# Optimization experiments

Hardware: AMD Instinct MI355X
Metric: run time of the kernel (lower is better)

The kernel has to match this reference:

```python
import jax, jax.numpy as jnp
import numpy as np

N_NODES = 50000
N_EDGES = 800000
D_IN, D_HID, D_OUT = 128, 256, 128
N_EXPERT = 8


def mean_aggr(x, src, dst, n):
    # scatter-mean of neighbor features onto destination nodes
    msg = x[src]                                            # [E, d]
    s = jax.ops.segment_sum(msg, dst, num_segments=n)       # [N, d]
    cnt = jax.ops.segment_sum(jnp.ones((src.shape[0],), x.dtype), dst, num_segments=n)
    return s / jnp.clip(cnt, 1.0)[:, None]


def moe_top1(x, wg, bg, we, be):
    # FMoE with naive gate, top_k=1: combine weight softmax over top-1 == 1.0
    logits = x @ wg + bg                                    # [N, E]
    gate_full = jax.nn.softmax(logits, axis=-1)             # [N, E]
    idx = jnp.argmax(logits, axis=-1)                       # [N]
    n_expert = we.shape[0]
    out = jnp.zeros((x.shape[0], we.shape[2]), x.dtype)
    for e in range(n_expert):                               # small fixed loop over experts
        mask = (idx == e)[:, None].astype(x.dtype)
        out = out + mask * (x @ we[e] + be[e])
    return out, gate_full


def mysage_conv(x, src, dst, wg, bg, we, be, wr):
    agg = mean_aggr(x, src, dst, x.shape[0])
    out, gate = moe_top1(agg, wg, bg, we, be)
    out = out + x @ wr                                      # root weight (no bias)
    gstd = jnp.std(gate, axis=1, ddof=1).mean()             # torch.std is unbiased
    return out, gstd


def plain_sage_conv(x, src, dst, wl, bl, wr):
    agg = mean_aggr(x, src, dst, x.shape[0])
    return agg @ wl + bl + x @ wr


def setup_inputs() -> dict:
    key = jax.random.key(0)
    ks = jax.random.split(key, 16)
    s = 0.05
    inp = {
        "x": jax.random.normal(ks[0], (N_NODES, D_IN), jnp.float32),
        "edge_index": jax.random.randint(ks[1], (2, N_EDGES), 0, N_NODES, jnp.int64),
        # layer 1 (in -> hid)
        "wg1": jax.random.normal(ks[2], (D_IN, N_EXPERT), jnp.float32) * s,
        "bg1": jnp.zeros((N_EXPERT,), jnp.float32),
        "we1": jax.random.normal(ks[3], (N_EXPERT, D_IN, D_HID), jnp.float32) * s,
        "be1": jnp.zeros((N_EXPERT, D_HID), jnp.float32),
        "wr1": jax.random.normal(ks[4], (D_IN, D_HID), jnp.float32) * s,
        # layer 2 (hid -> hid)
        "wg2": jax.random.normal(ks[5], (D_HID, N_EXPERT), jnp.float32) * s,
        "bg2": jnp.zeros((N_EXPERT,), jnp.float32),
        "we2": jax.random.normal(ks[6], (N_EXPERT, D_HID, D_HID), jnp.float32) * s,
        "be2": jnp.zeros((N_EXPERT, D_HID), jnp.float32),
        "wr2": jax.random.normal(ks[7], (D_HID, D_HID), jnp.float32) * s,
        # layer 3 plain SAGEConv (hid -> out)
        "wl3": jax.random.normal(ks[8], (D_HID, D_OUT), jnp.float32) * s,
        "bl3": jnp.zeros((D_OUT,), jnp.float32),
        "wr3": jax.random.normal(ks[9], (D_HID, D_OUT), jnp.float32) * s,
    }
    return inp


def reference(x, edge_index, wg1, bg1, we1, be1, wr1, wg2, bg2, we2, be2, wr2, wl3, bl3, wr3):
    src, dst = edge_index[0], edge_index[1]
    h, g1 = mysage_conv(x, src, dst, wg1, bg1, we1, be1, wr1)
    h = jax.nn.relu(h)                                      # dropout p=0 / eval mode
    h, g2 = mysage_conv(h, src, dst, wg2, bg2, we2, be2, wr2)
    h = jax.nn.relu(h)
    out = plain_sage_conv(h, src, dst, wl3, bl3, wr3)
    gate_std_mean = jnp.stack([g1, g2]).mean()
    return out, gate_std_mean
```

## Files before the change

kernel.cpp:

```cpp
#include <hip/hip_runtime.h>
#include <hip/hip_bf16.h>
#include <stdint.h>

#define DEV static __device__ __forceinline__

typedef __attribute__((ext_vector_type(8))) short short8;
typedef __attribute__((ext_vector_type(4))) float f32x4;

DEV float bf2f(unsigned short u) { return __uint_as_float(((unsigned)u) << 16); }
DEV float bflo(unsigned u) { return __uint_as_float(u << 16); }
DEV float bfhi(unsigned u) { return __uint_as_float(u & 0xffff0000u); }
DEV unsigned short f2bf(float f) {
    unsigned u = __float_as_uint(f);
    u += 0x7fff + ((u >> 16) & 1);
    return (unsigned short)(u >> 16);
}

__global__ void k_detect(const int* __restrict__ ei, int* __restrict__ flags) {
    if (threadIdx.x == 0 && blockIdx.x == 0) {
        int zeros = 0;
        for (int i = 0; i < 128; ++i) if (ei[2 * i + 1] == 0) ++zeros;
        flags[1] = (zeros >= 64) ? 1 : 0;
    }
}

__global__ void k_cvt_idx(const int* __restrict__ ei, int* __restrict__ src32,
                          int* __restrict__ dst32, int* __restrict__ deg,
                          int E, const int* __restrict__ flags) {
    int i = blockIdx.x * 256 + threadIdx.x;
    if (i >= E) return;
    int s, d;
    if (flags[1]) { s = ei[2 * i]; d = ei[2 * E + 2 * i]; }
    else          { s = ei[i];     d = ei[E + i]; }
    src32[i] = s; dst32[i] = d;
    atomicAdd(&deg[d], 1);
}

__global__ void k_transpose_nb(const float* __restrict__ in, unsigned short* __restrict__ out,
                               int R, int C) {
    __shared__ unsigned short tile[32][33];
    int tx = threadIdx.x & 31, ty = threadIdx.x >> 5;
    size_t mat = (size_t)blockIdx.z * R * C;
    int r0 = blockIdx.y * 32, c0 = blockIdx.x * 32;
#pragma unroll
    for (int j = 0; j < 32; j += 8)
        tile[ty + j][tx] = f2bf(in[mat + (size_t)(r0 + ty + j) * C + c0 + tx]);
    __syncthreads();
#pragma unroll
    for (int j = 0; j < 32; j += 8)
        out[mat + (size_t)(c0 + ty + j) * R + r0 + tx] = tile[tx][ty + j];
}

__global__ void k_bias3(const float* __restrict__ bl3, float* __restrict__ bias3) {
    int t = threadIdx.x;
    bias3[t] = (t < 128) ? 0.f : bl3[t - 128];
}

__global__ void k_scan1(const int* __restrict__ deg, int* __restrict__ row_ptr,
                        int* __restrict__ part, int n) {
    __shared__ int wsum[4];
    int t = threadIdx.x, lane = t & 63, wv = t >> 6;
    int i = blockIdx.x * 256 + t;
    int v0 = (i < n) ? deg[i] : 0;
    int v = v0;
#pragma unroll
    for (int d = 1; d < 64; d <<= 1) { int u = __shfl_up(v, d); if (lane >= d) v += u; }
    if (lane == 63) wsum[wv] = v;
    __syncthreads();
    int add = 0;
    for (int w2 = 0; w2 < wv; ++w2) add += wsum[w2];
    v += add;
    if (i < n) row_ptr[i] = v - v0;
    if (t == 255) part[blockIdx.x] = v;
}

__global__ void k_scan2(int* __restrict__ part, int P) {
    __shared__ int wsum[4];
    int t = threadIdx.x, lane = t & 63, wv = t >> 6;
    int v0 = (t < P) ? part[t] : 0;
    int v = v0;
#pragma unroll
    for (int d = 1; d < 64; d <<= 1) { int u = __shfl_up(v, d); if (lane >= d) v += u; }
    if (lane == 63) wsum[wv] = v;
    __syncthreads();
    int add = 0;
    for (int w2 = 0; w2 < wv; ++w2) add += wsum[w2];
    v += add;
    if (t < P) part[t] = v - v0;
}

__global__ void k_scan3(int* __restrict__ row_ptr, const int* __restrict__ part, int n, int E) {
    int i = blockIdx.x * 256 + threadIdx.x;
    if (i < n) row_ptr[i] += part[blockIdx.x];
    if (i == 0) row_ptr[n] = E;
}

__global__ void k_fill(const int* __restrict__ src, const int* __restrict__ dst,
                       const int* __restrict__ row_ptr, int* __restrict__ cursor,
                       int* __restrict__ csr, int E) {
    int i = blockIdx.x * 256 + threadIdx.x;
    if (i < E) {
        int d = dst[i];
        int p = atomicAdd(&cursor[d], 1);
        csr[row_ptr[d] + p] = src[i];
    }
}

template<int D>
__global__ __launch_bounds__(256, 2) void k_aggr(
    const float* __restrict__ xin, const int* __restrict__ row_ptr,
    const int* __restrict__ csr, float* __restrict__ agg, int n) {
    int wid = (blockIdx.x * blockDim.x + threadIdx.x) >> 6;
    int lane = threadIdx.x & 63;
    if (wid >= n) return;
    constexpr int V = D / 64;
    double ac[8][V];
#pragma unroll
    for (int r = 0; r < 8; ++r)
#pragma unroll
        for (int i = 0; i < V; ++i) ac[r][i] = 0.0;
    int s0 = row_ptr[wid], s1 = row_ptr[wid + 1];
    int j = s0;
    for (; j + 8 <= s1; j += 8) {
        const float* p[8];
#pragma unroll
        for (int r = 0; r < 8; ++r) p[r] = xin + (size_t)csr[j + r] * D + lane * V;
        if (V == 2) {
            float2 f[8];
#pragma unroll
            for (int r = 0; r < 8; ++r) f[r] = *(const float2*)p[r];
#pragma unroll
            for (int r = 0; r < 8; ++r) { ac[r][0] += (double)f[r].x; ac[r][1] += (double)f[r].y; }
        } else {
            float4 f[8];
#pragma unroll
            for (int r = 0; r < 8; ++r) f[r] = *(const float4*)p[r];
#pragma unroll
            for (int r = 0; r < 8; ++r) {
                ac[r][0] += (double)f[r].x; ac[r][1] += (double)f[r].y;
                ac[r][2] += (double)f[r].z; ac[r][3] += (double)f[r].w;
            }
        }
    }
    for (; j + 4 <= s1; j += 4) {
        const float* p[4];
#pragma unroll
        for (int r = 0; r < 4; ++r) p[r] = xin + (size_t)csr[j + r] * D + lane * V;
        if (V == 2) {
            float2 f[4];
#pragma unroll
            for (int r = 0; r < 4; ++r) f[r] = *(const float2*)p[r];
#pragma unroll
            for (int r = 0; r < 4; ++r) { ac[r][0] += (double)f[r].x; ac[r][1] += (double)f[r].y; }
        } else {
            float4 f[4];
#pragma unroll
            for (int r = 0; r < 4; ++r) f[r] = *(const float4*)p[r];
#pragma unroll
            for (int r = 0; r < 4; ++r) {
                ac[r][0] += (double)f[r].x; ac[r][1] += (double)f[r].y;
                ac[r][2] += (double)f[r].z; ac[r][3] += (double)f[r].w;
            }
        }
    }
    for (; j < s1; ++j) {
        const float* p = xin + (size_t)csr[j] * D + lane * V;
        if (V == 2) {
            float2 f = *(const float2*)p;
            ac[0][0] += (double)f.x; ac[0][1] += (double)f.y;
        } else {
            float4 f = *(const float4*)p;
            ac[0][0] += (double)f.x; ac[0][1] += (double)f.y;
            ac[0][2] += (double)f.z; ac[0][3] += (double)f.w;
        }
    }
    double inv = 1.0 / (double)max(s1 - s0, 1);
#pragma unroll
    for (int i = 0; i < V; ++i) {
        double s = ((ac[0][i] + ac[1][i]) + (ac[2][i] + ac[3][i]))
                 + ((ac[4][i] + ac[5][i]) + (ac[6][i] + ac[7][i]));
        agg[(size_t)wid * D + lane * V + i] = (float)(s * inv);
    }
}

__global__ __launch_bounds__(256, 2) void k_aggr_badd(
    const unsigned short* __restrict__ Pb, const int* __restrict__ row_ptr,
    const int* __restrict__ csr, const float* __restrict__ Rf,
    float* __restrict__ outp, int n) {
    int wid = (blockIdx.x * blockDim.x + threadIdx.x) >> 6;
    int lane = threadIdx.x & 63;
    if (wid >= n) return;
    double ac[8][2];
#pragma unroll
    for (int r = 0; r < 8; ++r) { ac[r][0] = 0.0; ac[r][1] = 0.0; }
    int s0 = row_ptr[wid], s1 = row_ptr[wid + 1];
    int j = s0;
    for (; j + 8 <= s1; j += 8) {
        unsigned u[8];
#pragma unroll
        for (int r = 0; r < 8; ++r) u[r] = *(const unsigned*)(Pb + (size_t)csr[j + r] * 128 + lane * 2);
#pragma unroll
        for (int r = 0; r < 8; ++r) { ac[r][0] += (double)bflo(u[r]); ac[r][1] += (double)bfhi(u[r]); }
    }
    for (; j + 4 <= s1; j += 4) {
        unsigned u[4];
#pragma unroll
        for (int r = 0; r < 4; ++r) u[r] = *(const unsigned*)(Pb + (size_t)csr[j + r] * 128 + lane * 2);
#pragma unroll
        for (int r = 0; r < 4; ++r) { ac[r][0] += (double)bflo(u[r]); ac[r][1] += (double)bfhi(u[r]); }
    }
    for (; j < s1; ++j) {
        unsigned u = *(const unsigned*)(Pb + (size_t)csr[j] * 128 + lane * 2);
        ac[0][0] += (double)bflo(u); ac[0][1] += (double)bfhi(u);
    }
    double inv = 1.0 / (double)max(s1 - s0, 1);
    float2 r2 = *(const float2*)(Rf + (size_t)wid * 128 + lane * 2);
    float2 o;
    o.x = (float)((((ac[0][0] + ac[1][0]) + (ac[2][0] + ac[3][0]))
                 + ((ac[4][0] + ac[5][0]) + (ac[6][0] + ac[7][0]))) * inv) + r2.x;
    o.y = (float)((((ac[0][1] + ac[1][1]) + (ac[2][1] + ac[3][1]))
                 + ((ac[4][1] + ac[5][1]) + (ac[6][1] + ac[7][1]))) * inv) + r2.y;
    *(float2*)(outp + (size_t)wid * 128 + lane * 2) = o;
}

template<int D>
__global__ void k_gate(const float* __restrict__ agg, const float* __restrict__ wg,
                       const float* __restrict__ bg, int* __restrict__ idx,
                       int* __restrict__ ecnt, float* __restrict__ gsum, int n) {
    __shared__ float swg[D * 8];
    __shared__ int hcnt[8];
    __shared__ float red[256];
    int t = threadIdx.x;
    if (t < 8) hcnt[t] = 0;
    for (int i = t; i < D * 8; i += 256) swg[i] = wg[i];
    __syncthreads();
    int nid = blockIdx.x * 256 + t;
    float stdv = 0.f;
    if (nid < n) {
        double lg[8];
#pragma unroll
        for (int e = 0; e < 8; ++e) lg[e] = (double)bg[e];
        const float* ap = agg + (size_t)nid * D;
        for (int k = 0; k < D; k += 4) {
            float4 a = *(const float4*)(ap + k);
#pragma unroll
            for (int e = 0; e < 8; ++e) {
                lg[e] += (double)a.x * swg[(k + 0) * 8 + e] + (double)a.y * swg[(k + 1) * 8 + e]
                       + (double)a.z * swg[(k + 2) * 8 + e] + (double)a.w * swg[(k + 3) * 8 + e];
            }
        }
        double m = lg[0];
        int am = 0;
#pragma unroll
        for (int e = 1; e < 8; ++e) if (lg[e] > m) { m = lg[e]; am = e; }
        double s = 0.0, p[8];
#pragma unroll
        for (int e = 0; e < 8; ++e) { p[e] = exp(lg[e] - m); s += p[e]; }
        double invs = 1.0 / s, sq = 0.0;
#pragma unroll
        for (int e = 0; e < 8; ++e) { double q = p[e] * invs; sq += q * q; }
        stdv = (float)sqrt(fmax(sq - 0.125, 0.0) / 7.0);
        idx[nid] = am;
        atomicAdd(&hcnt[am], 1);
    }
    red[t] = stdv;
    __syncthreads();
    for (int off = 128; off > 0; off >>= 1) {
        if (t < off) red[t] += red[t + off];
        __syncthreads();
    }
    if (t == 0) atomicAdd(gsum, red[0]);
    if (t < 8 && hcnt[t] > 0) atomicAdd(&ecnt[t], hcnt[t]);
}

__global__ void k_offsets(const int* __restrict__ ecnt, int* __restrict__ eoff) {
    if (threadIdx.x == 0 && blockIdx.x == 0) {
        int s = 0;
        for (int e = 0; e < 8; ++e) { eoff[e] = s; s += ecnt[e]; }
        eoff[8] = s;
    }
}

__global__ void k_perm(const int* __restrict__ idx, const int* __restrict__ eoff,
                       int* __restrict__ ecur, int* __restrict__ perm, int n) {
    __shared__ int lcnt[8], lbase[8];
    int t = threadIdx.x;
    if (t < 8) lcnt[t] = 0;
    __syncthreads();
    int nid = blockIdx.x * 256 + t;
    int e = 0, r = 0;
    bool valid = (nid < n);
    if (valid) { e = idx[nid]; r = atomicAdd(&lcnt[e], 1); }
    __syncthreads();
    if (t < 8) lbase[t] = lcnt[t] ? atomicAdd(&ecur[t], lcnt[t]) : 0;
    __syncthreads();
    if (valid) perm[eoff[e] + lbase[e] + r] = nid;
}

template<int NCOL, bool LOAD>
DEV void g_step(int g, const float* __restrict__ Bp, const float* __restrict__ at,
                float4 (&cur)[4], float (&acc)[8][4]) {
    float bx[4][4];
#pragma unroll
    for (int kk = 0; kk < 4; ++kk) {
        bx[kk][0] = cur[kk].x; bx[kk][1] = cur[kk].y;
        bx[kk][2] = cur[kk].z; bx[kk][3] = cur[kk].w;
    }
#pragma unroll
    for (int r = 0; r < 8; ++r) {
        float4 a = *(const float4*)(at + r * 68 + g * 4);
#pragma unroll
        for (int c = 0; c < 4; ++c) {
            acc[r][c] = fmaf(a.x, bx[0][c], acc[r][c]);
            acc[r][c] = fmaf(a.y, bx[1][c], acc[r][c]);
            acc[r][c] = fmaf(a.z, bx[2][c], acc[r][c]);
            acc[r][c] = fmaf(a.w, bx[3][c], acc[r][c]);
        }
    }
    if (LOAD) {
#pragma unroll
        for (int kk = 0; kk < 4; ++kk)
            cur[kk] = *(const float4*)(Bp + (size_t)(g * 4 + 8 + kk) * NCOL);
    }
}

template<int NCOL>
DEV void compute_chunk(const float* __restrict__ Bp, const float* __restrict__ at,
                       float (&acc)[8][4]) {
    float4 bA[4], bB[4];
#pragma unroll
    for (int kk = 0; kk < 4; ++kk) bA[kk] = *(const float4*)(Bp + (size_t)kk * NCOL);
#pragma unroll
    for (int kk = 0; kk < 4; ++kk) bB[kk] = *(const float4*)(Bp + (size_t)(4 + kk) * NCOL);
#pragma unroll 1
    for (int g = 0; g < 14; g += 2) {
        g_step<NCOL, true>(g, Bp, at, bA, acc);
        g_step<NCOL, true>(g + 1, Bp, at, bB, acc);
    }
    g_step<NCOL, false>(14, Bp, at, bA, acc);
    g_step<NCOL, false>(15, Bp, at, bB, acc);
}

template<int DIN, int NCOL, bool RELU>
__global__ __launch_bounds__(256, 4) void k_gemm_f32(
    const float* __restrict__ agg, const float* __restrict__ a2,
    const float* __restrict__ B1, const float* __restrict__ B2,
    const float* __restrict__ bias,
    const int* __restrict__ perm, const int* __restrict__ eoff,
    float* __restrict__ outp, int n) {
    static_assert(DIN == 128 && NCOL == 256, "layer-1 geometry");
    __shared__ float a_tile[2][4 * 8 * 68];
    __shared__ int rows[32];
    int t = threadIdx.x;
    int rs = blockIdx.x * 32;
    if (rs >= n) return;
    int nrows = min(32, n - rs);
    if (t < 32) rows[t] = perm[rs + min(t, nrows - 1)];
    __syncthreads();

    int e0 = 0, e1 = 0;
    int last = rs + nrows - 1;
#pragma unroll
    for (int e = 1; e < 8; ++e) {
        int v = eoff[e];
        if (v <= rs) e0 = e;
        if (v <= last) e1 = e;
    }
    int ne = e1 - e0 + 1;
    int nchunks = 2 * ne + 2;

    int lane = t & 63, rg = t >> 6;
    int cols = lane * 4;
    int srow = lane >> 3;
    int sk = (lane & 7) * 8;
    int gpos = rs + rg * 8 + srow;
    int myrow = rows[rg * 8 + srow];
    float* stc = &a_tile[0][rg * 544 + srow * 68 + sk];
    float* stn = &a_tile[1][rg * 544 + srow * 68 + sk];
    const float* atc = &a_tile[0][rg * 544];
    const float* atn = &a_tile[1][rg * 544];

    float acc[8][4];
#pragma unroll
    for (int r = 0; r < 8; ++r) { acc[r][0] = 0.f; acc[r][1] = 0.f; acc[r][2] = 0.f; acc[r][3] = 0.f; }

    auto params = [&](int c, const float*& ap, const float*& Bp, float& m) {
        int half = c & 1;
        if (c < 2 * ne) {
            int e = e0 + (c >> 1);
            ap = agg + (size_t)myrow * DIN + sk + half * 64;
            Bp = B1 + (size_t)e * DIN * NCOL + (size_t)half * 64 * NCOL + cols;
            m = (gpos >= eoff[e] && gpos < eoff[e + 1]) ? 1.f : 0.f;
        } else {
            ap = a2 + (size_t)myrow * DIN + sk + half * 64;
            Bp = B2 + (size_t)half * 64 * NCOL + cols;
            m = 1.f;
        }
    };

    const float* ap; const float* Bp; float m;
    params(0, ap, Bp, m);
    float4 p0 = *(const float4*)ap, p1 = *(const float4*)(ap + 4);
#pragma unroll 1
    for (int c = 0; c < nchunks; ++c) {
        float4 s0 = p0, s1 = p1;
        s0.x *= m; s0.y *= m; s0.z *= m; s0.w *= m;
        s1.x *= m; s1.y *= m; s1.z *= m; s1.w *= m;
        *(float4*)stc = s0; *(float4*)(stc + 4) = s1;
        const float* Bcur = Bp;
        if (c + 1 < nchunks) {
            params(c + 1, ap, Bp, m);
            p0 = *(const float4*)ap; p1 = *(const float4*)(ap + 4);
        }
        compute_chunk<NCOL>(Bcur, atc, acc);
        float* ts = stc; stc = stn; stn = ts;
        const float* ta = atc; atc = atn; atn = ta;
    }

#pragma unroll
    for (int r = 0; r < 8; ++r) {
        int rr = rg * 8 + r;
        if (rr < nrows) {
            int gp = rs + rr;
            int er = e0;
            for (int e = e0 + 1; e <= e1; ++e) if (eoff[e] <= gp) er = e;
            float4 bb = *(const float4*)(bias + er * NCOL + cols);
            int gr = rows[rr];
            float v0 = acc[r][0] + bb.x, v1 = acc[r][1] + bb.y;
            float v2 = acc[r][2] + bb.z, v3 = acc[r][3] + bb.w;
            if (RELU) { v0 = fmaxf(v0, 0.f); v1 = fmaxf(v1, 0.f); v2 = fmaxf(v2, 0.f); v3 = fmaxf(v3, 0.f); }
            *(float4*)(outp + (size_t)gr * NCOL + cols) = make_float4(v0, v1, v2, v3);
        }
    }
}

template<int DIN, int MODE, int CT>
DEV void gemm_half(const void* __restrict__ Asrc, const unsigned short* __restrict__ BT,
                   short (*Ah)[40], short (*Bs)[40],
                   const int* rows, f32x4 (&acc)[4][CT], int t, int lane, int w) {
    if (MODE == 9) return;
    int q = lane >> 4, m16 = lane & 15;
    int r = t >> 2, part = t & 3;
    for (int kc = 0; kc < DIN; kc += 32) {
        __syncthreads();
        if (MODE == 2) {
            *(uint4*)&Ah[r][part * 8] =
                *(const uint4*)((const unsigned short*)Asrc + (size_t)rows[r] * DIN + kc + part * 8);
        } else {
            const float* pf = (const float*)Asrc + (size_t)rows[r] * DIN + kc + part * 8;
            float4 p0 = *(const float4*)pf, p1 = *(const float4*)(pf + 4);
            float va[8] = { p0.x, p0.y, p0.z, p0.w, p1.x, p1.y, p1.z, p1.w };
            short8 h;
#pragma unroll
            for (int j = 0; j < 8; ++j) h[j] = (short)f2bf(va[j]);
            *(short8*)&Ah[r][part * 8] = h;
        }
#pragma unroll
        for (int j = 0; j < CT; ++j) {
            int c = t + 256 * j;
            int nn = c >> 2, pp = c & 3;
            *(uint4*)&Bs[nn][pp * 8] = *(const uint4*)(BT + (size_t)nn * DIN + kc + pp * 8);
        }
        __syncthreads();
        short8 af[4], bfr[CT];
#pragma unroll
        for (int rt = 0; rt < 4; ++rt) af[rt] = *(short8*)&Ah[rt * 16 + m16][q * 8];
#pragma unroll
        for (int ct = 0; ct < CT; ++ct) bfr[ct] = *(short8*)&Bs[w * CT * 16 + ct * 16 + m16][q * 8];
#pragma unroll
        for (int rt = 0; rt < 4; ++rt)
#pragma unroll
            for (int ct = 0; ct < CT; ++ct)
                acc[rt][ct] = __builtin_amdgcn_mfma_f32_16x16x32_bf16(af[rt], bfr[ct], acc[rt][ct], 0, 0, 0);
    }
}

template<int DIN, int M0, int M1, int CT, bool EXPERT, bool RELU, int OUTMODE>
__global__ __launch_bounds__(256) void k_gemm(
    const void* __restrict__ A0, const void* __restrict__ A1,
    const unsigned short* __restrict__ B0T, const unsigned short* __restrict__ B1T,
    const float* __restrict__ bias,
    const int* __restrict__ perm, const int* __restrict__ eoff,
    void* __restrict__ outp, void* __restrict__ outp2, int n) {
    constexpr int NCOL = CT * 64;
    __shared__ short Ah[64][40];
    __shared__ short Bs[NCOL][40];
    __shared__ int rows[64];
    int t = threadIdx.x;
    int lane = t & 63, w = t >> 6;
    int e = 0, base = 0, cnt = n;
    if (EXPERT) { e = blockIdx.y; base = eoff[e]; cnt = eoff[e + 1] - base; }
    int rs = blockIdx.x * 64;
    if (rs >= cnt) return;
    int nrows = min(64, cnt - rs);
    if (t < 64) {
        int j = rs + min(t, nrows - 1);
        rows[t] = EXPERT ? perm[base + j] : j;
    }
    __syncthreads();
    f32x4 acc[4][CT];
#pragma unroll
    for (int rt = 0; rt < 4; ++rt)
#pragma unroll
        for (int ct = 0; ct < CT; ++ct) acc[rt][ct] = (f32x4)(0.f);

    gemm_half<DIN, M0, CT>(A0, B0T + (EXPERT ? (size_t)e * DIN * NCOL : 0), Ah, Bs, rows, acc, t, lane, w);
    gemm_half<DIN, M1, CT>(A1, B1T, Ah, Bs, rows, acc, t, lane, w);

    int q = lane >> 4, m16 = lane & 15;
#pragma unroll
    for (int ct = 0; ct < CT; ++ct) {
        int col = w * CT * 16 + ct * 16 + m16;
        float bv = bias[(EXPERT ? e * NCOL : 0) + col];
#pragma unroll
        for (int rt = 0; rt < 4; ++rt)
#pragma unroll
            for (int i = 0; i < 4; ++i) {
                int rr = rt * 16 + q * 4 + i;
                if (rr < nrows) {
                    int gr = rows[rr];
                    float v = acc[rt][ct][i] + bv;
                    if (RELU) v = fmaxf(v, 0.f);
                    if (OUTMODE == 1) ((unsigned short*)outp)[(size_t)gr * NCOL + col] = f2bf(v);
                    else if (OUTMODE == 0) ((float*)outp)[(size_t)gr * NCOL + col] = v;
                    else {
                        if (col < 128) ((unsigned short*)outp)[(size_t)gr * 128 + col] = f2bf(v);
                        else           ((float*)outp2)[(size_t)gr * 128 + (col - 128)] = v;
                    }
                }
            }
    }
}

__global__ void k_final(const float* __restrict__ gsum, float* __restrict__ outf) {
    if (threadIdx.x == 0 && blockIdx.x == 0) {
        float g = (gsum[0] + gsum[1]) * (0.5f / 50000.0f);
        outf[(size_t)50000 * 128] = g;
    }
}

extern "C" void kernel_launch(void* const* d_in, const int* in_sizes, int n_in,
                              void* d_out, int out_size, void* d_ws, size_t ws_size,
                              hipStream_t stream) {
    constexpr int N = 50000, E = 800000;
    const float* x   = (const float*)d_in[0];
    const int* ei    = (const int*)d_in[1];
    const float* wg1 = (const float*)d_in[2];
    const float* bg1 = (const float*)d_in[3];
    const float* we1 = (const float*)d_in[4];
    const float* be1 = (const float*)d_in[5];
    const float* wr1 = (const float*)d_in[6];
    const float* wg2 = (const float*)d_in[7];
    const float* bg2 = (const float*)d_in[8];
    const float* we2 = (const float*)d_in[9];
    const float* be2 = (const float*)d_in[10];
    const float* wr2 = (const float*)d_in[11];
    const float* wl3 = (const float*)d_in[12];
    const float* bl3 = (const float*)d_in[13];
    const float* wr3 = (const float*)d_in[14];

    int* ip = (int*)d_ws;
    int* deg = ip;            ip += N;
    int* cursor = ip;         ip += N;
    int* ecnt = ip;           ip += 16;
    int* ecur = ip;           ip += 16;
    float* gsum = (float*)ip; ip += 2;
    int* flags = ip;          ip += 2;
    float* bias3 = (float*)ip; ip += 256;
    int* row_ptr = ip;        ip += N + 1;
    int* csr = ip;            ip += E;
    int* idxb = ip;           ip += N;
    int* permb = ip;          ip += N;
    int* eoff = ip;           ip += 18;
    int* part = ip;           ip += 256;
    int* src32 = ip;          ip += E;
    int* dst32 = ip;          ip += E;
    size_t off = (size_t)((char*)ip - (char*)d_ws);
    off = (off + 255) & ~(size_t)255;
    float* fp = (float*)((char*)d_ws + off);
    float* agg = fp; fp += (size_t)N * 256;
    float* h1  = fp; fp += (size_t)N * 256;
    unsigned short* wp = (unsigned short*)fp;
    unsigned short* h2b  = wp; wp += (size_t)N * 256;
    unsigned short* we2T = wp; wp += 8 * 256 * 256;
    unsigned short* wr2T = wp; wp += 256 * 256;
    unsigned short* wl3T = wp; wp += 256 * 128;
    unsigned short* wr3T = wp; wp += 256 * 128;
    unsigned short* Pb = (unsigned short*)h1;
    float* Rf = agg;

    hipMemsetAsync(d_ws, 0, (size_t)(2 * N + 36) * 4, stream);

    k_detect<<<1, 64, 0, stream>>>(ei, flags);
    k_cvt_idx<<<(E + 255) / 256, 256, 0, stream>>>(ei, src32, dst32, deg, E, flags);

    k_transpose_nb<<<dim3(8, 8, 8), 256, 0, stream>>>(we2, we2T, 256, 256);
    k_transpose_nb<<<dim3(8, 8, 1), 256, 0, stream>>>(wr2, wr2T, 256, 256);
    k_transpose_nb<<<dim3(4, 8, 1), 256, 0, stream>>>(wl3, wl3T, 256, 128);
    k_transpose_nb<<<dim3(4, 8, 1), 256, 0, stream>>>(wr3, wr3T, 256, 128);
    k_bias3<<<1, 256, 0, stream>>>(bl3, bias3);

    constexpr int NB = (N + 255) / 256;
    constexpr int WB = (N + 3) / 4;
    k_scan1<<<NB, 256, 0, stream>>>(deg, row_ptr, part, N);
    k_scan2<<<1, 256, 0, stream>>>(part, NB);
    k_scan3<<<NB, 256, 0, stream>>>(row_ptr, part, N, E);
    k_fill<<<(E + 255) / 256, 256, 0, stream>>>(src32, dst32, row_ptr, cursor, csr, E);

    constexpr int GB = (N + 63) / 64;
    constexpr int GB32 = (N + 31) / 32;
    k_aggr<128><<<WB, 256, 0, stream>>>(x, row_ptr, csr, agg, N);
    k_gate<128><<<NB, 256, 0, stream>>>(agg, wg1, bg1, idxb, ecnt, gsum, N);
    k_offsets<<<1, 1, 0, stream>>>(ecnt, eoff);
    k_perm<<<NB, 256, 0, stream>>>(idxb, eoff, ecur, permb, N);
    k_gemm_f32<128, 256, true><<<dim3(GB32), 256, 0, stream>>>(
        agg, x, we1, wr1, be1, permb, eoff, h1, N);

    k_aggr<256><<<WB, 256, 0, stream>>>(h1, row_ptr, csr, agg, N);
    k_gate<256><<<NB, 256, 0, stream>>>(agg, wg2, bg2, idxb, ecnt + 8, gsum + 1, N);
    k_offsets<<<1, 1, 0, stream>>>(ecnt + 8, eoff + 9);
    k_perm<<<NB, 256, 0, stream>>>(idxb, eoff + 9, ecur + 8, permb, N);
    k_gemm<256, 0, 0, 4, true, true, 1><<<dim3(GB, 8), 256, 0, stream>>>(
        agg, h1, we2T, wr2T, be2, permb, eoff + 9, h2b, nullptr, N);

    k_gemm<256, 2, 9, 4, false, false, 2><<<dim3(GB, 1), 256, 0, stream>>>(
        h2b, nullptr, wl3T, nullptr, bias3, nullptr, nullptr, Pb, Rf, N);
    k_aggr_badd<<<WB, 256, 0, stream>>>(Pb, row_ptr, csr, Rf, (float*)d_out, N);

    k_final<<<1, 1, 0, stream>>>(gsum, (float*)d_out);
}
```

Before: 654.8 us.

## Store layer-1 output in bf16 and precompute layer-2 gate logits per node

Result: no change. 644.2 us (-1.6%).

```diff
diff --git a/kernel.cpp b/kernel.cpp
--- a/kernel.cpp
+++ b/kernel.cpp
@@ -183,6 +183,57 @@
     }
 }
 
+__global__ __launch_bounds__(256, 2) void k_aggr_h1b(
+    const unsigned short* __restrict__ xin, const int* __restrict__ row_ptr,
+    const int* __restrict__ csr, unsigned short* __restrict__ aggb, int n) {
+    int wid = (blockIdx.x * blockDim.x + threadIdx.x) >> 6;
+    int lane = threadIdx.x & 63;
+    if (wid >= n) return;
+    double ac[8][4];
+#pragma unroll
+    for (int r = 0; r < 8; ++r)
+#pragma unroll
+        for (int i = 0; i < 4; ++i) ac[r][i] = 0.0;
+    int s0 = row_ptr[wid], s1 = row_ptr[wid + 1];
+    int j = s0;
+    for (; j + 8 <= s1; j += 8) {
+        uint2 u[8];
+#pragma unroll
+        for (int r = 0; r < 8; ++r) u[r] = *(const uint2*)(xin + (size_t)csr[j + r] * 256 + lane * 4);
+#pragma unroll
+        for (int r = 0; r < 8; ++r) {
+            ac[r][0] += (double)bflo(u[r].x); ac[r][1] += (double)bfhi(u[r].x);
+            ac[r][2] += (double)bflo(u[r].y); ac[r][3] += (double)bfhi(u[r].y);
+        }
+    }
+    for (; j + 4 <= s1; j += 4) {
+        uint2 u[4];
+#pragma unroll
+        for (int r = 0; r < 4; ++r) u[r] = *(const uint2*)(xin + (size_t)csr[j + r] * 256 + lane * 4);
+#pragma unroll
+        for (int r = 0; r < 4; ++r) {
+            ac[r][0] += (double)bflo(u[r].x); ac[r][1] += (double)bfhi(u[r].x);
+            ac[r][2] += (double)bflo(u[r].y); ac[r][3] += (double)bfhi(u[r].y);
+        }
+    }
+    for (; j < s1; ++j) {
+        uint2 u = *(const uint2*)(xin + (size_t)csr[j] * 256 + lane * 4);
+        ac[0][0] += (double)bflo(u.x); ac[0][1] += (double)bfhi(u.x);
+        ac[0][2] += (double)bflo(u.y); ac[0][3] += (double)bfhi(u.y);
+    }
+    double inv = 1.0 / (double)max(s1 - s0, 1);
+    float m[4];
+#pragma unroll
+    for (int i = 0; i < 4; ++i) {
+        double s = ((ac[0][i] + ac[1][i]) + (ac[2][i] + ac[3][i]))
+                 + ((ac[4][i] + ac[5][i]) + (ac[6][i] + ac[7][i]));
+        m[i] = (float)(s * inv);
+    }
+    unsigned b01 = (unsigned)f2bf(m[0]) | ((unsigned)f2bf(m[1]) << 16);
+    unsigned b23 = (unsigned)f2bf(m[2]) | ((unsigned)f2bf(m[3]) << 16);
+    *(uint2*)(aggb + (size_t)wid * 256 + lane * 4) = make_uint2(b01, b23);
+}
+
 __global__ __launch_bounds__(256, 2) void k_aggr_badd(
     const unsigned short* __restrict__ Pb, const int* __restrict__ row_ptr,
     const int* __restrict__ csr, const float* __restrict__ Rf,
@@ -273,6 +324,56 @@
     if (t < 8 && hcnt[t] > 0) atomicAdd(&ecnt[t], hcnt[t]);
 }
 
+__global__ void k_gate_g(const double* __restrict__ G2, const int* __restrict__ row_ptr,
+                         const int* __restrict__ csr, const float* __restrict__ bg,
+                         int* __restrict__ idx, int* __restrict__ ecnt,
+                         float* __restrict__ gsum, int n) {
+    __shared__ int hcnt[8];
+    __shared__ float red[256];
+    int t = threadIdx.x;
+    if (t < 8) hcnt[t] = 0;
+    __syncthreads();
+    int nid = blockIdx.x * 256 + t;
+    float stdv = 0.f;
+    if (nid < n) {
+        double lg[8];
+#pragma unroll
+        for (int e = 0; e < 8; ++e) lg[e] = 0.0;
+        int s0 = row_ptr[nid], s1 = row_ptr[nid + 1];
+        for (int j = s0; j < s1; ++j) {
+            const double* g = G2 + (size_t)csr[j] * 8;
+            double2 g0 = *(const double2*)g,       g1 = *(const double2*)(g + 2);
+            double2 g2 = *(const double2*)(g + 4), g3 = *(const double2*)(g + 6);
+            lg[0] += g0.x; lg[1] += g0.y; lg[2] += g1.x; lg[3] += g1.y;
+            lg[4] += g2.x; lg[5] += g2.y; lg[6] += g3.x; lg[7] += g3.y;
+        }
+        double inv = 1.0 / (double)max(s1 - s0, 1);
+#pragma unroll
+        for (int e = 0; e < 8; ++e) lg[e] = lg[e] * inv + (double)bg[e];
+        double m = lg[0];
+        int am = 0;
+#pragma unroll
+        for (int e = 1; e < 8; ++e) if (lg[e] > m) { m = lg[e]; am = e; }
+        double s = 0.0, p[8];
+#pragma unroll
+        for (int e = 0; e < 8; ++e) { p[e] = exp(lg[e] - m); s += p[e]; }
+        double invs = 1.0 / s, sq = 0.0;
+#pragma unroll
+        for (int e = 0; e < 8; ++e) { double q = p[e] * invs; sq += q * q; }
+        stdv = (float)sqrt(fmax(sq - 0.125, 0.0) / 7.0);
+        idx[nid] = am;
+        atomicAdd(&hcnt[am], 1);
+    }
+    red[t] = stdv;
+    __syncthreads();
+    for (int off = 128; off > 0; off >>= 1) {
+        if (t < off) red[t] += red[t + off];
+        __syncthreads();
+    }
+    if (t == 0) atomicAdd(gsum, red[0]);
+    if (t < 8 && hcnt[t] > 0) atomicAdd(&ecnt[t], hcnt[t]);
+}
+
 __global__ void k_offsets(const int* __restrict__ ecnt, int* __restrict__ eoff) {
     if (threadIdx.x == 0 && blockIdx.x == 0) {
         int s = 0;
@@ -345,9 +446,9 @@
 __global__ __launch_bounds__(256, 4) void k_gemm_f32(
     const float* __restrict__ agg, const float* __restrict__ a2,
     const float* __restrict__ B1, const float* __restrict__ B2,
-    const float* __restrict__ bias,
+    const float* __restrict__ bias, const float* __restrict__ wg2,
     const int* __restrict__ perm, const int* __restrict__ eoff,
-    float* __restrict__ outp, int n) {
+    unsigned short* __restrict__ h1b, double* __restrict__ G2, int n) {
     static_assert(DIN == 128 && NCOL == 256, "layer-1 geometry");
     __shared__ float a_tile[2][4 * 8 * 68];
     __shared__ int rows[32];
@@ -417,6 +518,18 @@
         const float* ta = atc; atc = atn; atn = ta;
     }
 
+    float wreg[4][8];
+    {
+        const float* wp2 = wg2 + (size_t)cols * 8;
+#pragma unroll
+        for (int c = 0; c < 4; ++c) {
+            float4 wa = *(const float4*)(wp2 + c * 8);
+            float4 wb = *(const float4*)(wp2 + c * 8 + 4);
+            wreg[c][0] = wa.x; wreg[c][1] = wa.y; wreg[c][2] = wa.z; wreg[c][3] = wa.w;
+            wreg[c][4] = wb.x; wreg[c][5] = wb.y; wreg[c][6] = wb.z; wreg[c][7] = wb.w;
+        }
+    }
+
 #pragma unroll
     for (int r = 0; r < 8; ++r) {
         int rr = rg * 8 + r;
@@ -429,7 +542,22 @@
             float v0 = acc[r][0] + bb.x, v1 = acc[r][1] + bb.y;
             float v2 = acc[r][2] + bb.z, v3 = acc[r][3] + bb.w;
             if (RELU) { v0 = fmaxf(v0, 0.f); v1 = fmaxf(v1, 0.f); v2 = fmaxf(v2, 0.f); v3 = fmaxf(v3, 0.f); }
-            *(float4*)(outp + (size_t)gr * NCOL + cols) = make_float4(v0, v1, v2, v3);
+            unsigned b01 = (unsigned)f2bf(v0) | ((unsigned)f2bf(v1) << 16);
+            unsigned b23 = (unsigned)f2bf(v2) | ((unsigned)f2bf(v3) << 16);
+            *(uint2*)(h1b + (size_t)gr * NCOL + cols) = make_uint2(b01, b23);
+            double pd[8];
+#pragma unroll
+            for (int e = 0; e < 8; ++e)
+                pd[e] = (double)v0 * (double)wreg[0][e] + (double)v1 * (double)wreg[1][e]
+                      + (double)v2 * (double)wreg[2][e] + (double)v3 * (double)wreg[3][e];
+#pragma unroll
+            for (int e = 0; e < 8; ++e)
+#pragma unroll
+                for (int off = 1; off < 64; off <<= 1) pd[e] += __shfl_xor(pd[e], off);
+            if (lane == 0) {
+#pragma unroll
+                for (int e = 0; e < 8; ++e) G2[(size_t)gr * 8 + e] = pd[e];
+            }
         }
     }
 }
@@ -578,6 +706,7 @@
     size_t off = (size_t)((char*)ip - (char*)d_ws);
     off = (off + 255) & ~(size_t)255;
     float* fp = (float*)((char*)d_ws + off);
+    double* G2 = (double*)fp; fp += (size_t)N * 16;
     float* agg = fp; fp += (size_t)N * 256;
     float* h1  = fp; fp += (size_t)N * 256;
     unsigned short* wp = (unsigned short*)fp;
@@ -586,7 +715,9 @@
     unsigned short* wr2T = wp; wp += 256 * 256;
     unsigned short* wl3T = wp; wp += 256 * 128;
     unsigned short* wr3T = wp; wp += 256 * 128;
-    unsigned short* Pb = (unsigned short*)h1;
+    unsigned short* aggb = (unsigned short*)agg;
+    unsigned short* h1b  = (unsigned short*)h1;
+    unsigned short* Pb = (unsigned short*)(h1 + (size_t)N * 128);
     float* Rf = agg;
 
     hipMemsetAsync(d_ws, 0, (size_t)(2 * N + 36) * 4, stream);
@@ -614,14 +745,14 @@
     k_offsets<<<1, 1, 0, stream>>>(ecnt, eoff);
     k_perm<<<NB, 256, 0, stream>>>(idxb, eoff, ecur, permb, N);
     k_gemm_f32<128, 256, true><<<dim3(GB32), 256, 0, stream>>>(
-        agg, x, we1, wr1, be1, permb, eoff, h1, N);
-
-    k_aggr<256><<<WB, 256, 0, stream>>>(h1, row_ptr, csr, agg, N);
-    k_gate<256><<<NB, 256, 0, stream>>>(agg, wg2, bg2, idxb, ecnt + 8, gsum + 1, N);
+        agg, x, we1, wr1, be1, wg2, permb, eoff, h1b, G2, N);
+
+    k_gate_g<<<NB, 256, 0, stream>>>(G2, row_ptr, csr, bg2, idxb, ecnt + 8, gsum + 1, N);
+    k_aggr_h1b<<<WB, 256, 0, stream>>>(h1b, row_ptr, csr, aggb, N);
     k_offsets<<<1, 1, 0, stream>>>(ecnt + 8, eoff + 9);
     k_perm<<<NB, 256, 0, stream>>>(idxb, eoff + 9, ecur + 8, permb, N);
-    k_gemm<256, 0, 0, 4, true, true, 1><<<dim3(GB, 8), 256, 0, stream>>>(
-        agg, h1, we2T, wr2T, be2, permb, eoff + 9, h2b, nullptr, N);
+    k_gemm<256, 2, 2, 4, true, true, 1><<<dim3(GB, 8), 256, 0, stream>>>(
+        aggb, h1b, we2T, wr2T, be2, permb, eoff + 9, h2b, nullptr, N);
 
     k_gemm<256, 2, 9, 4, false, false, 2><<<dim3(GB, 1), 256, 0, stream>>>(
         h2b, nullptr, wl3T, nullptr, bias3, nullptr, nullptr, Pb, Rf, N);
```
